# Optimization experiments

Hardware: AMD Instinct MI355X
Metric: run time of the kernel (lower is better)

The kernel has to match this reference:

```python
import jax, jax.numpy as jnp
import numpy as np

B, A, D = 1024, 200, 128
H = 8
DH = D // H
TANH_CLIP = 10.0


def setup_inputs() -> dict:
    key = jax.random.key(0)
    k = jax.random.split(key, 8)
    agent_embd = jax.random.normal(k[0], (B, A, D), dtype=jnp.float32)
    # old_action must be a permutation per row (no revisits under the mask)
    old_action = jax.vmap(lambda kk: jax.random.permutation(kk, A))(
        jax.random.split(k[1], B)).astype(jnp.int32)
    s = 0.02
    W_placeholder = jax.random.uniform(k[2], (D,), jnp.float32, -1.0, 1.0)
    W_node = jax.random.normal(k[3], (D, 3 * D), jnp.float32) * s   # project_node_embeddings
    W_fixed = jax.random.normal(k[4], (D, D), jnp.float32) * s      # project_fixed_context
    W_step = jax.random.normal(k[5], (D, D), jnp.float32) * s       # project_step_context
    W_out = jax.random.normal(k[6], (D, D), jnp.float32) * s        # project_out
    return {"agent_embd": agent_embd, "old_action": old_action,
            "W_placeholder": W_placeholder, "W_node": W_node,
            "W_fixed": W_fixed, "W_step": W_step, "W_out": W_out}


def _decode(agent_embd, old_action, W_placeholder, W_node, W_fixed, W_step, W_out):
    b_, a_, d_ = agent_embd.shape
    inv_sqrt_dh = np.float32(1.0 / np.sqrt(DH))
    inv_sqrt_d = np.float32(1.0 / np.sqrt(d_))
    batch_ix = jnp.arange(b_)

    # _precompute: fixed context + per-head K/V + logit keys
    graph_embed = agent_embd.mean(axis=1)                      # [B, D]
    fixed_ctx = graph_embed @ W_fixed                          # [B, D]
    proj = agent_embd @ W_node                                 # [B, A, 3D]
    gK, gV, logit_K = jnp.split(proj, 3, axis=-1)              # each [B, A, D]
    gK = gK.reshape(b_, a_, H, DH).transpose(2, 0, 1, 3)       # [H, B, A, dh]
    gV = gV.reshape(b_, a_, H, DH).transpose(2, 0, 1, 3)       # [H, B, A, dh]

    def step(carry, xs):
        mask, prev = carry                                     # [B, A] bool, [B] int
        i, act = xs
        gathered = agent_embd[batch_ix, prev]                  # [B, D]
        step_ctx = jnp.where(i == 0, W_placeholder[None, :], gathered)
        query = fixed_ctx + step_ctx @ W_step                  # [B, D]
        mask = jnp.where(i > 0, mask.at[batch_ix, prev].set(True), mask)

        Q = query.reshape(b_, H, DH).transpose(1, 0, 2)        # [H, B, dh]
        compat = jnp.einsum('hbd,hbad->hba', Q, gK) * inv_sqrt_dh
        compat = jnp.where(mask[None, :, :], -jnp.inf, compat)  # mask_inner
        attn = jax.nn.softmax(compat, axis=-1)                 # [H, B, A]
        heads = jnp.einsum('hba,hbad->hbd', attn, gV)          # [H, B, dh]
        glimpse = heads.transpose(1, 0, 2).reshape(b_, d_) @ W_out  # [B, D]

        logits = jnp.einsum('bd,bad->ba', glimpse, logit_K) * inv_sqrt_d
        logits = jnp.tanh(logits) * TANH_CLIP
        logits = jnp.where(mask, -jnp.inf, logits)             # mask_logits
        log_p = jax.nn.log_softmax(logits, axis=-1)            # [B, A]
        lp_sel = log_p[batch_ix, act]                          # [B]
        return (mask, act), lp_sel

    mask0 = jnp.zeros((b_, a_), dtype=bool)
    prev0 = jnp.zeros((b_,), dtype=old_action.dtype)
    xs = (jnp.arange(a_), old_action.T)
    _, lps = jax.lax.scan(step, (mask0, prev0), xs)            # lps: [A, B]
    return old_action, lps.sum(axis=0)


def reference(agent_embd, old_action, W_placeholder, W_node, W_fixed, W_step, W_out):
    return _decode(agent_embd, old_action, W_placeholder, W_node, W_fixed, W_step, W_out)
```

## Files before the change

### kernel.cpp

```cpp
#include <hip/hip_runtime.h>
#include <cstdint>
#include <cstddef>

#define BB 1024
#define AA 200
#define DD 128
#define HH 8
#define N3 384

typedef unsigned short u16;
typedef unsigned int u32;
typedef __attribute__((ext_vector_type(8))) short bf16x8;
typedef __attribute__((ext_vector_type(4))) float f32x4;

__device__ __forceinline__ float bf2f(u16 v){ return __uint_as_float(((u32)v) << 16); }
__device__ __forceinline__ u16 f2bf(float f){
  u32 u = __float_as_uint(f);
  u32 r = u + 0x7fffu + ((u >> 16) & 1u);
  return (u16)(r >> 16);
}
__device__ __forceinline__ u16 f2bf_trunc(float f){
  return (u16)(__float_as_uint(f) >> 16);
}
__device__ __forceinline__ bf16x8 pack8(float4 a, float4 b){
  bf16x8 o;
  o[0] = (short)f2bf(a.x); o[1] = (short)f2bf(a.y);
  o[2] = (short)f2bf(a.z); o[3] = (short)f2bf(a.w);
  o[4] = (short)f2bf(b.x); o[5] = (short)f2bf(b.y);
  o[6] = (short)f2bf(b.z); o[7] = (short)f2bf(b.w);
  return o;
}

__global__ void k_act_rank(const int* __restrict__ oa, float* __restrict__ out0,
                           int* __restrict__ rank){
  int m = blockIdx.x * 256 + threadIdx.x;
  if (m >= BB*AA) return;
  int v = oa[m];
  out0[m] = (float)v;
  int b = m / AA;
  int j = m - b*AA;
  rank[b*AA + v] = j;
}

__global__ void k_prep(const float* __restrict__ Wn, const float* __restrict__ Ws,
                       const float* __restrict__ Wo,
                       u16* __restrict__ WnT, u16* __restrict__ WsT,
                       u16* __restrict__ WoT){
  int idx = blockIdx.x * 256 + threadIdx.x;
  if (idx < 49152){
    int n = idx >> 7, k = idx & 127;
    WnT[idx] = f2bf(Wn[k*N3 + n]);
  } else if (idx < 65536){
    int j = idx - 49152;
    int n = j >> 7, k = j & 127;
    WsT[j] = f2bf(Ws[k*DD + n]);
  } else if (idx < 81920){
    int j = idx - 65536;
    int n = j >> 7, k = j & 127;
    WoT[j] = f2bf(Wo[k*DD + n]);
  }
}

__global__ void k_fixed(const float* __restrict__ E, const float* __restrict__ Wf,
                        float* __restrict__ fixedc){
  int b = blockIdx.x;
  int d = threadIdx.x;
  __shared__ float ge[DD];
  const float* Eb = E + (size_t)b*AA*DD;
  float s = 0.f;
  for (int a = 0; a < AA; ++a) s += Eb[a*DD + d];
  ge[d] = s * (1.0f/AA);
  __syncthreads();
  float acc = 0.f;
  for (int k = 0; k < DD; ++k) acc = fmaf(ge[k], Wf[k*DD + d], acc);
  fixedc[b*DD + d] = acc;
}

__global__ __launch_bounds__(256) void k_proj_mfma(const float* __restrict__ E,
                                                   const u16* __restrict__ WnT,
                                                   u16* __restrict__ proj){
  const int t = threadIdx.x;
  const int w = t >> 6, L = t & 63;
  const int l16 = L & 15, lq = L >> 4;
  const int m0 = blockIdx.x * 128;
  const int n0 = blockIdx.y * 128;
  const int row0 = m0 + w*32;

  f32x4 acc[2][8] = {};
  const float* Arow0 = E + (size_t)(row0 + l16)*DD;
  const float* Arow1 = Arow0 + (size_t)16*DD;
  #pragma unroll
  for (int ks = 0; ks < 4; ++ks){
    int ko = ks*32 + lq*8;
    bf16x8 a0 = pack8(*(const float4*)(Arow0 + ko), *(const float4*)(Arow0 + ko + 4));
    bf16x8 a1 = pack8(*(const float4*)(Arow1 + ko), *(const float4*)(Arow1 + ko + 4));
    #pragma unroll
    for (int nt = 0; nt < 8; ++nt){
      union { uint4 u; bf16x8 v; } bb;
      bb.u = *(const uint4*)(WnT + (size_t)(n0 + nt*16 + l16)*DD + ko);
      acc[0][nt] = __builtin_amdgcn_mfma_f32_16x16x32_bf16(a0, bb.v, acc[0][nt], 0, 0, 0);
      acc[1][nt] = __builtin_amdgcn_mfma_f32_16x16x32_bf16(a1, bb.v, acc[1][nt], 0, 0, 0);
    }
  }
  #pragma unroll
  for (int mt = 0; mt < 2; ++mt)
    #pragma unroll
    for (int r = 0; r < 4; ++r){
      int row = row0 + mt*16 + lq*4 + r;
      u16* dst = proj + (size_t)row*N3 + n0;
      #pragma unroll
      for (int nt = 0; nt < 8; ++nt)
        dst[nt*16 + l16] = f2bf(acc[mt][nt][r]);
    }
}

__global__ __launch_bounds__(256) void k_query_mfma(const float* __restrict__ E,
                                                    const int* __restrict__ oa,
                                                    const float* __restrict__ Wp,
                                                    const u16* __restrict__ WsT,
                                                    const float* __restrict__ fixedc,
                                                    u16* __restrict__ qhg){
  const int t = threadIdx.x;
  const int w = t >> 6, L = t & 63;
  const int l16 = L & 15, lq = L >> 4;
  const int m0 = blockIdx.x * 128;
  const int row0 = m0 + w*32;

  const float* src[2];
  #pragma unroll
  for (int mt = 0; mt < 2; ++mt){
    int q = row0 + mt*16 + l16;
    int b = q / AA, i = q - b*AA;
    src[mt] = (i == 0) ? Wp : (E + (size_t)(b*AA + oa[b*AA + i - 1])*DD);
  }

  f32x4 acc[2][8] = {};
  #pragma unroll
  for (int ks = 0; ks < 4; ++ks){
    int ko = ks*32 + lq*8;
    bf16x8 a0 = pack8(*(const float4*)(src[0] + ko), *(const float4*)(src[0] + ko + 4));
    bf16x8 a1 = pack8(*(const float4*)(src[1] + ko), *(const float4*)(src[1] + ko + 4));
    #pragma unroll
    for (int nt = 0; nt < 8; ++nt){
      union { uint4 u; bf16x8 v; } bb;
      bb.u = *(const uint4*)(WsT + (size_t)(nt*16 + l16)*DD + ko);
      acc[0][nt] = __builtin_amdgcn_mfma_f32_16x16x32_bf16(a0, bb.v, acc[0][nt], 0, 0, 0);
      acc[1][nt] = __builtin_amdgcn_mfma_f32_16x16x32_bf16(a1, bb.v, acc[1][nt], 0, 0, 0);
    }
  }
  #pragma unroll
  for (int mt = 0; mt < 2; ++mt)
    #pragma unroll
    for (int r = 0; r < 4; ++r){
      int row = row0 + mt*16 + lq*4 + r;
      int b = row / AA;
      const float* fc = fixedc + (size_t)b*DD;
      u16* dst = qhg + (size_t)row*DD;
      #pragma unroll
      for (int nt = 0; nt < 8; ++nt)
        dst[nt*16 + l16] = f2bf((acc[mt][nt][r] + fc[nt*16 + l16]) * 0.25f);
    }
}

#define KSTR 24
#define VSTR 232
__global__ __launch_bounds__(256) void k_attn(const u16* __restrict__ proj,
                                              const int* __restrict__ rank,
                                              u16* __restrict__ qhg){
  __shared__ __align__(16) u16 KL[208*KSTR];
  __shared__ __align__(16) u16 VT[16*VSTR];
  __shared__ __align__(16) u16 P [4][16*VSTR];
  const int b = blockIdx.x;
  const int h = blockIdx.y;
  const int t = threadIdx.x;
  const int w = t >> 6, L = t & 63;
  const int l16 = L & 15, lq = L >> 4;

  for (int idx = t; idx < 208*KSTR; idx += 256) KL[idx] = 0;
  for (int idx = t; idx < 16*VSTR; idx += 256) VT[idx] = 0;
  {
    u16* Pw = P[w];
    for (int idx = L; idx < 16*VSTR; idx += 64) Pw[idx] = 0;
  }

  if (t < AA){
    const u16* src = proj + ((size_t)(b*AA + t))*N3 + h*16;
    uint4 k0 = *(const uint4*)(src);
    uint4 k1 = *(const uint4*)(src + 8);
    *(uint4*)&KL[t*KSTR]     = k0;
    *(uint4*)&KL[t*KSTR + 8] = k1;
    const u16* sv = src + 128;
    u16 d16[16];
    *(uint4*)(d16)   = *(const uint4*)(sv);
    *(uint4*)(d16+8) = *(const uint4*)(sv+8);
    #pragma unroll
    for (int d = 0; d < 16; ++d) VT[d*VSTR + t] = d16[d];
  }

  int ra[13];
  #pragma unroll
  for (int at = 0; at < 13; ++at){
    int a = at*16 + l16;
    ra[at] = (a < AA) ? rank[b*AA + a] : -1;
  }
  __syncthreads();

  u16* Qbase = qhg + (size_t)b*AA*DD + h*16;
  u16* Pw = P[w];

  const bf16x8 zf = {0,0,0,0,0,0,0,0};
  for (int it = w; it < 13; it += 4){
    bf16x8 qf = zf;
    int qi = it*16 + l16;
    if (lq < 2 && qi < AA){
      union { uint4 u; bf16x8 v; } tmp;
      tmp.u = *(const uint4*)(Qbase + (size_t)qi*DD + lq*8);
      qf = tmp.v;
    }
    f32x4 S[13];
    #pragma unroll
    for (int at = 0; at < 13; ++at){
      bf16x8 kf = zf;
      if (lq < 2){
        union { uint4 u; bf16x8 v; } tmp;
        tmp.u = *(const uint4*)&KL[(at*16 + l16)*KSTR + lq*8];
        kf = tmp.v;
      }
      f32x4 z = {0.f,0.f,0.f,0.f};
      S[at] = __builtin_amdgcn_mfma_f32_16x16x32_bf16(qf, kf, z, 0, 0, 0);
    }
    #pragma unroll
    for (int at = 0; at < 13; ++at)
      #pragma unroll
      for (int r = 0; r < 4; ++r){
        int i = it*16 + lq*4 + r;
        S[at][r] = (ra[at] < i) ? -__builtin_inff() : S[at][r];
      }
    float inv[4];
    #pragma unroll
    for (int r = 0; r < 4; ++r){
      float m = S[0][r];
      #pragma unroll
      for (int at = 1; at < 13; ++at) m = fmaxf(m, S[at][r]);
      #pragma unroll
      for (int off = 1; off < 16; off <<= 1) m = fmaxf(m, __shfl_xor(m, off));
      float sum = 0.f;
      #pragma unroll
      for (int at = 0; at < 13; ++at){
        float e = __expf(S[at][r] - m);
        S[at][r] = e; sum += e;
      }
      #pragma unroll
      for (int off = 1; off < 16; off <<= 1) sum += __shfl_xor(sum, off);
      inv[r] = 1.0f / sum;
    }
    #pragma unroll
    for (int at = 0; at < 13; ++at)
      #pragma unroll
      for (int r = 0; r < 4; ++r)
        Pw[(lq*4 + r)*VSTR + at*16 + l16] = f2bf_trunc(S[at][r]);
    f32x4 acc = {0.f,0.f,0.f,0.f};
    #pragma unroll
    for (int kb = 0; kb < 7; ++kb){
      union { uint4 u; bf16x8 v; } pa, vb;
      pa.u = *(const uint4*)&Pw[l16*VSTR + kb*32 + lq*8];
      vb.u = *(const uint4*)&VT[l16*VSTR + kb*32 + lq*8];
      acc = __builtin_amdgcn_mfma_f32_16x16x32_bf16(pa.v, vb.v, acc, 0, 0, 0);
    }
    #pragma unroll
    for (int r = 0; r < 4; ++r){
      int i = it*16 + lq*4 + r;
      if (i < AA) Qbase[(size_t)i*DD + l16] = f2bf(acc[r] * inv[r]);
    }
  }
}

__global__ __launch_bounds__(256) void k_glimpse_mfma(const u16* __restrict__ qhg,
                                                      const u16* __restrict__ WoT,
                                                      u16* __restrict__ proj){
  const int t = threadIdx.x;
  const int w = t >> 6, L = t & 63;
  const int l16 = L & 15, lq = L >> 4;
  const int m0 = blockIdx.x * 128;
  const int row0 = m0 + w*32;

  f32x4 acc[2][8] = {};
  const u16* Arow0 = qhg + (size_t)(row0 + l16)*DD;
  const u16* Arow1 = Arow0 + (size_t)16*DD;
  #pragma unroll
  for (int ks = 0; ks < 4; ++ks){
    int ko = ks*32 + lq*8;
    union { uint4 u; bf16x8 v; } a0, a1;
    a0.u = *(const uint4*)(Arow0 + ko);
    a1.u = *(const uint4*)(Arow1 + ko);
    #pragma unroll
    for (int nt = 0; nt < 8; ++nt){
      union { uint4 u; bf16x8 v; } bb;
      bb.u = *(const uint4*)(WoT + (size_t)(nt*16 + l16)*DD + ko);
      acc[0][nt] = __builtin_amdgcn_mfma_f32_16x16x32_bf16(a0.v, bb.v, acc[0][nt], 0, 0, 0);
      acc[1][nt] = __builtin_amdgcn_mfma_f32_16x16x32_bf16(a1.v, bb.v, acc[1][nt], 0, 0, 0);
    }
  }
  #pragma unroll
  for (int mt = 0; mt < 2; ++mt)
    #pragma unroll
    for (int r = 0; r < 4; ++r){
      int row = row0 + mt*16 + lq*4 + r;
      u16* dst = proj + (size_t)row*N3;
      #pragma unroll
      for (int nt = 0; nt < 8; ++nt)
        dst[nt*16 + l16] = f2bf(acc[mt][nt][r]);
    }
}

__global__ __launch_bounds__(256) void k_logits(const u16* __restrict__ proj,
                                                const int* __restrict__ rank,
                                                const int* __restrict__ oa,
                                                float* __restrict__ outlps){
  __shared__ float red[4];
  const int b = blockIdx.x;
  const int t = threadIdx.x;
  const int w = t >> 6, L = t & 63;
  const int l16 = L & 15, lq = L >> 4;
  const float inv_sqrt_d = 0.08838834764831843f;

  const u16* Gbase  = proj + (size_t)b*AA*N3;
  const u16* LKbase = Gbase + 256;

  int ra[13];
  #pragma unroll
  for (int at = 0; at < 13; ++at){
    int a = at*16 + l16;
    ra[at] = (a < AA) ? rank[b*AA + a] : -1;
  }

  float lp_part = 0.f;

  for (int it = w; it < 13; it += 4){
    bf16x8 af[4];
    {
      const u16* arow = Gbase + (size_t)(it*16 + l16)*N3;
      #pragma unroll
      for (int kb = 0; kb < 4; ++kb){
        union { uint4 u; bf16x8 v; } tmp;
        tmp.u = *(const uint4*)(arow + kb*32 + lq*8);
        af[kb] = tmp.v;
      }
    }
    f32x4 S[13];
    #pragma unroll
    for (int at = 0; at < 13; ++at){
      const u16* brow = LKbase + (size_t)(at*16 + l16)*N3;
      f32x4 acc = {0.f,0.f,0.f,0.f};
      #pragma unroll
      for (int kb = 0; kb < 4; ++kb){
        union { uint4 u; bf16x8 v; } tmp;
        tmp.u = *(const uint4*)(brow + kb*32 + lq*8);
        acc = __builtin_amdgcn_mfma_f32_16x16x32_bf16(af[kb], tmp.v, acc, 0, 0, 0);
      }
      S[at] = acc;
    }
    #pragma unroll
    for (int at = 0; at < 13; ++at)
      #pragma unroll
      for (int r = 0; r < 4; ++r){
        int i = it*16 + lq*4 + r;
        float x = S[at][r] * inv_sqrt_d;
        float e = __expf(2.0f*x);
        float th = 1.0f - 2.0f/(e + 1.0f);
        S[at][r] = (ra[at] < i) ? -__builtin_inff() : 10.0f*th;
      }
    #pragma unroll
    for (int r = 0; r < 4; ++r){
      int i = it*16 + lq*4 + r;
      float m = S[0][r];
      #pragma unroll
      for (int at = 1; at < 13; ++at) m = fmaxf(m, S[at][r]);
      #pragma unroll
      for (int off = 1; off < 16; off <<= 1) m = fmaxf(m, __shfl_xor(m, off));
      float sum = 0.f;
      #pragma unroll
      for (int at = 0; at < 13; ++at) sum += __expf(S[at][r] - m);
      #pragma unroll
      for (int off = 1; off < 16; off <<= 1) sum += __shfl_xor(sum, off);
      if (i < AA){
        float lse = m + __logf(sum);
        int act = oa[b*AA + i];
        if ((act & 15) == l16){
          int at0 = act >> 4;
          #pragma unroll
          for (int at = 0; at < 13; ++at)
            if (at == at0) lp_part += S[at][r] - lse;
        }
      }
    }
  }
  #pragma unroll
  for (int off = 1; off < 64; off <<= 1) lp_part += __shfl_xor(lp_part, off);
  if (L == 0) red[w] = lp_part;
  __syncthreads();
  if (t == 0) outlps[b] = red[0] + red[1] + red[2] + red[3];
}

extern "C" void kernel_launch(void* const* d_in, const int* in_sizes, int n_in,
                              void* d_out, int out_size, void* d_ws, size_t ws_size,
                              hipStream_t stream){
  const float* E  = (const float*)d_in[0];
  const int*   oa = (const int*)d_in[1];
  const float* Wp = (const float*)d_in[2];
  const float* Wn = (const float*)d_in[3];
  const float* Wf = (const float*)d_in[4];
  const float* Ws = (const float*)d_in[5];
  const float* Wo = (const float*)d_in[6];
  float* out = (float*)d_out;

  char* ws = (char*)d_ws;
  int*   rank   = (int*)ws;
  float* fixedc = (float*)(ws + 819200);
  u16*   proj   = (u16*)(ws + 1343488);
  u16*   qhg    = (u16*)(ws + 158629888);
  u16*   WnT    = (u16*)(ws + 211058688);
  u16*   WsT    = (u16*)(ws + 211156992);
  u16*   WoT    = (u16*)(ws + 211189760);

  k_act_rank<<<dim3((BB*AA)/256), 256, 0, stream>>>(oa, out, rank);
  k_prep<<<dim3(320), 256, 0, stream>>>(Wn, Ws, Wo, WnT, WsT, WoT);
  k_fixed<<<dim3(BB), 128, 0, stream>>>(E, Wf, fixedc);
  k_proj_mfma<<<dim3((BB*AA)/128, N3/128), 256, 0, stream>>>(E, WnT, proj);
  k_query_mfma<<<dim3((BB*AA)/128), 256, 0, stream>>>(E, oa, Wp, WsT, fixedc, qhg);
  k_attn<<<dim3(BB, HH), 256, 0, stream>>>(proj, rank, qhg);
  k_glimpse_mfma<<<dim3((BB*AA)/128), 256, 0, stream>>>(qhg, WoT, proj);
  k_logits<<<dim3(BB), 256, 0, stream>>>(proj, rank, oa, out + BB*AA);
}
```

Baseline: 737.5 us.

## Transpose attention MFMA to keep softmax probabilities in registers, drop LDS P buffer

Swaps the MFMA operand order in the attention kernel so scores come out transposed (keys along registers, queries along lanes). The softmax row reduction then mostly happens inside each thread, and the probabilities are packed straight into the PV MFMA operand, with no round trip through the per-wave LDS P buffer. Ranks are packed as bytes for cheaper mask checks, and the full LDS zero-fill is cut down to the padding regions. In exchange it uses half-filled K=32 MFMAs (13 for PV instead of 7) and rounds P to bf16 with rounding instead of truncation.

```diff
diff --git a/kernel.cpp b/kernel.cpp
--- a/kernel.cpp
+++ b/kernel.cpp
@@ -19,8 +19,8 @@
   u32 r = u + 0x7fffu + ((u >> 16) & 1u);
   return (u16)(r >> 16);
 }
-__device__ __forceinline__ u16 f2bf_trunc(float f){
-  return (u16)(__float_as_uint(f) >> 16);
+__device__ __forceinline__ u32 pack2(float lo, float hi){
+  return (u32)f2bf(lo) | ((u32)f2bf(hi) << 16);
 }
 __device__ __forceinline__ bf16x8 pack8(float4 a, float4 b){
   bf16x8 o;
@@ -169,19 +169,14 @@
                                               u16* __restrict__ qhg){
   __shared__ __align__(16) u16 KL[208*KSTR];
   __shared__ __align__(16) u16 VT[16*VSTR];
-  __shared__ __align__(16) u16 P [4][16*VSTR];
   const int b = blockIdx.x;
   const int h = blockIdx.y;
   const int t = threadIdx.x;
   const int w = t >> 6, L = t & 63;
   const int l16 = L & 15, lq = L >> 4;
 
-  for (int idx = t; idx < 208*KSTR; idx += 256) KL[idx] = 0;
-  for (int idx = t; idx < 16*VSTR; idx += 256) VT[idx] = 0;
-  {
-    u16* Pw = P[w];
-    for (int idx = L; idx < 16*VSTR; idx += 64) Pw[idx] = 0;
-  }
+  if (t < 192) KL[200*KSTR + t] = 0;
+  if (t < 128){ int d = t >> 3, c = t & 7; VT[d*VSTR + 200 + c] = 0; }
 
   if (t < AA){
     const u16* src = proj + ((size_t)(b*AA + t))*N3 + h*16;
@@ -197,80 +192,90 @@
     for (int d = 0; d < 16; ++d) VT[d*VSTR + t] = d16[d];
   }
 
-  int ra[13];
+  u32 ra_pk[13];
   #pragma unroll
   for (int at = 0; at < 13; ++at){
-    int a = at*16 + l16;
-    ra[at] = (a < AA) ? rank[b*AA + a] : -1;
+    int a0 = at*16 + lq*4;
+    u32 p = 0;
+    if (a0 + 3 < AA){
+      int4 rv = *(const int4*)(rank + (size_t)b*AA + a0);
+      p = (u32)(rv.x+1) | ((u32)(rv.y+1)<<8) | ((u32)(rv.z+1)<<16) | ((u32)(rv.w+1)<<24);
+    }
+    ra_pk[at] = p;
   }
   __syncthreads();
 
   u16* Qbase = qhg + (size_t)b*AA*DD + h*16;
-  u16* Pw = P[w];
-
-  const bf16x8 zf = {0,0,0,0,0,0,0,0};
+  const float NEG_INF = -__builtin_inff();
+
   for (int it = w; it < 13; it += 4){
-    bf16x8 qf = zf;
-    int qi = it*16 + l16;
-    if (lq < 2 && qi < AA){
-      union { uint4 u; bf16x8 v; } tmp;
-      tmp.u = *(const uint4*)(Qbase + (size_t)qi*DD + lq*8);
-      qf = tmp.v;
-    }
+    const int qi = it*16 + l16;
+    union { uint4 u; bf16x8 v; } qf8;
+    qf8.u.x = 0; qf8.u.y = 0; qf8.u.z = 0; qf8.u.w = 0;
+    if (qi < AA){
+      uint2 q2 = *(const uint2*)(Qbase + (size_t)qi*DD + lq*4);
+      qf8.u.x = q2.x; qf8.u.y = q2.y;
+    }
+
     f32x4 S[13];
     #pragma unroll
     for (int at = 0; at < 13; ++at){
-      bf16x8 kf = zf;
-      if (lq < 2){
-        union { uint4 u; bf16x8 v; } tmp;
-        tmp.u = *(const uint4*)&KL[(at*16 + l16)*KSTR + lq*8];
-        kf = tmp.v;
-      }
+      union { uint4 u; bf16x8 v; } kf8;
+      uint2 k2 = *(const uint2*)&KL[(at*16 + l16)*KSTR + lq*4];
+      kf8.u.x = k2.x; kf8.u.y = k2.y; kf8.u.z = 0; kf8.u.w = 0;
       f32x4 z = {0.f,0.f,0.f,0.f};
-      S[at] = __builtin_amdgcn_mfma_f32_16x16x32_bf16(qf, kf, z, 0, 0, 0);
-    }
+      S[at] = __builtin_amdgcn_mfma_f32_16x16x32_bf16(kf8.v, qf8.v, z, 0, 0, 0);
+    }
+    const u32 iv = (u32)(qi + 1);
+    #pragma unroll
+    for (int at = 0; at < 13; ++at){
+      const u32 pk = ra_pk[at];
+      #pragma unroll
+      for (int r = 0; r < 4; ++r)
+        if (((pk >> (8*r)) & 0xFFu) < iv) S[at][r] = NEG_INF;
+    }
+    float mx[13];
     #pragma unroll
     for (int at = 0; at < 13; ++at)
-      #pragma unroll
-      for (int r = 0; r < 4; ++r){
-        int i = it*16 + lq*4 + r;
-        S[at][r] = (ra[at] < i) ? -__builtin_inff() : S[at][r];
-      }
-    float inv[4];
-    #pragma unroll
-    for (int r = 0; r < 4; ++r){
-      float m = S[0][r];
-      #pragma unroll
-      for (int at = 1; at < 13; ++at) m = fmaxf(m, S[at][r]);
-      #pragma unroll
-      for (int off = 1; off < 16; off <<= 1) m = fmaxf(m, __shfl_xor(m, off));
-      float sum = 0.f;
-      #pragma unroll
-      for (int at = 0; at < 13; ++at){
-        float e = __expf(S[at][r] - m);
-        S[at][r] = e; sum += e;
-      }
-      #pragma unroll
-      for (int off = 1; off < 16; off <<= 1) sum += __shfl_xor(sum, off);
-      inv[r] = 1.0f / sum;
-    }
-    #pragma unroll
-    for (int at = 0; at < 13; ++at)
-      #pragma unroll
-      for (int r = 0; r < 4; ++r)
-        Pw[(lq*4 + r)*VSTR + at*16 + l16] = f2bf_trunc(S[at][r]);
+      mx[at] = fmaxf(fmaxf(S[at][0], S[at][1]), fmaxf(S[at][2], S[at][3]));
+    float m01 = fmaxf(mx[0], mx[1]),  m23 = fmaxf(mx[2], mx[3]);
+    float m45 = fmaxf(mx[4], mx[5]),  m67 = fmaxf(mx[6], mx[7]);
+    float m89 = fmaxf(mx[8], mx[9]),  mab = fmaxf(mx[10], mx[11]);
+    float m = fmaxf(fmaxf(fmaxf(m01, m23), fmaxf(m45, m67)),
+                    fmaxf(fmaxf(m89, mab), mx[12]));
+    m = fmaxf(m, __shfl_xor(m, 16));
+    m = fmaxf(m, __shfl_xor(m, 32));
+    m = fmaxf(m, -1e30f);
+    float s0 = 0.f, s1 = 0.f, s2 = 0.f, s3 = 0.f;
+    #pragma unroll
+    for (int at = 0; at < 13; ++at){
+      float e0 = __expf(S[at][0] - m);
+      float e1 = __expf(S[at][1] - m);
+      float e2 = __expf(S[at][2] - m);
+      float e3 = __expf(S[at][3] - m);
+      S[at][0] = e0; S[at][1] = e1; S[at][2] = e2; S[at][3] = e3;
+      s0 += e0; s1 += e1; s2 += e2; s3 += e3;
+    }
+    float sum = (s0 + s1) + (s2 + s3);
+    sum += __shfl_xor(sum, 16);
+    sum += __shfl_xor(sum, 32);
+    float inv = 1.0f / sum;
     f32x4 acc = {0.f,0.f,0.f,0.f};
     #pragma unroll
-    for (int kb = 0; kb < 7; ++kb){
-      union { uint4 u; bf16x8 v; } pa, vb;
-      pa.u = *(const uint4*)&Pw[l16*VSTR + kb*32 + lq*8];
-      vb.u = *(const uint4*)&VT[l16*VSTR + kb*32 + lq*8];
-      acc = __builtin_amdgcn_mfma_f32_16x16x32_bf16(pa.v, vb.v, acc, 0, 0, 0);
-    }
-    #pragma unroll
-    for (int r = 0; r < 4; ++r){
-      int i = it*16 + lq*4 + r;
-      if (i < AA) Qbase[(size_t)i*DD + l16] = f2bf(acc[r] * inv[r]);
+    for (int kt = 0; kt < 13; ++kt){
+      union { uint4 u; bf16x8 v; } pa8, vb8;
+      pa8.u.x = pack2(S[kt][0], S[kt][1]);
+      pa8.u.y = pack2(S[kt][2], S[kt][3]);
+      pa8.u.z = 0; pa8.u.w = 0;
+      uint2 v2 = *(const uint2*)&VT[l16*VSTR + kt*16 + lq*4];
+      vb8.u.x = v2.x; vb8.u.y = v2.y; vb8.u.z = 0; vb8.u.w = 0;
+      acc = __builtin_amdgcn_mfma_f32_16x16x32_bf16(vb8.v, pa8.v, acc, 0, 0, 0);
+    }
+    if (qi < AA){
+      uint2 ov;
+      ov.x = pack2(acc[0]*inv, acc[1]*inv);
+      ov.y = pack2(acc[2]*inv, acc[3]*inv);
+      *(uint2*)(Qbase + (size_t)qi*DD + lq*4) = ov;
     }
   }
 }
```

Result: no change. 740.8 us (+0.5%).
